# Kernel tuning notes

Measured on AMD Instinct MI355X. Metric: run time of the kernel, lower is better.

## Reference

```python
import jax, jax.numpy as jnp
import numpy as np

IN, H, FC1, FC2, OUT = 3, 30, 64, 32, 1
B, T = 8192, 256


def _lstm_layer(xT, W_ih, W_hh, b_ih, b_hh):
    """xT: (T, B, Din). Returns (hidden sequence (T,B,H), final h (B,H)).
    PyTorch gate order: i, f, g, o."""
    # Precompute input contribution for all timesteps (one big GEMM).
    gx = jnp.einsum('tbd,gd->tbg', xT, W_ih) + b_ih + b_hh  # (T,B,4H)
    b = xT.shape[1]
    h0 = jnp.zeros((b, W_hh.shape[1]), xT.dtype)
    c0 = h0

    def step(carry, g):
        h, c = carry
        gates = g + h @ W_hh.T
        i, f, gg, o = jnp.split(gates, 4, axis=-1)
        i = jax.nn.sigmoid(i)
        f = jax.nn.sigmoid(f)
        gg = jnp.tanh(gg)
        o = jax.nn.sigmoid(o)
        c = f * c + i * gg
        h = o * jnp.tanh(c)
        return (h, c), h

    (h_n, _), ys = jax.lax.scan(step, (h0, c0), gx)
    return ys, h_n


def setup_inputs() -> dict:
    key = jax.random.key(0)
    ks = jax.random.split(key, 16)
    s = 0.18  # ~1/sqrt(hidden_size), matches PyTorch uniform init scale
    inp = {
        'x': jax.random.normal(ks[0], (B, T, IN), jnp.float32),
        'W_ih0': jax.random.normal(ks[1], (4 * H, IN), jnp.float32) * s,
        'W_hh0': jax.random.normal(ks[2], (4 * H, H), jnp.float32) * s,
        'b_ih0': jax.random.normal(ks[3], (4 * H,), jnp.float32) * s,
        'b_hh0': jax.random.normal(ks[4], (4 * H,), jnp.float32) * s,
        'W_ih1': jax.random.normal(ks[5], (4 * H, H), jnp.float32) * s,
        'W_hh1': jax.random.normal(ks[6], (4 * H, H), jnp.float32) * s,
        'b_ih1': jax.random.normal(ks[7], (4 * H,), jnp.float32) * s,
        'b_hh1': jax.random.normal(ks[8], (4 * H,), jnp.float32) * s,
        'W_fc1': jax.random.normal(ks[9], (FC1, H), jnp.float32) * s,
        'b_fc1': jax.random.normal(ks[10], (FC1,), jnp.float32) * s,
        'W_fc2': jax.random.normal(ks[11], (FC2, FC1), jnp.float32) * 0.125,
        'b_fc2': jax.random.normal(ks[12], (FC2,), jnp.float32) * 0.125,
        'W_fc3': jax.random.normal(ks[13], (OUT, FC2), jnp.float32) * 0.17,
        'b_fc3': jax.random.normal(ks[14], (OUT,), jnp.float32) * 0.17,
    }
    return inp


def reference(x, W_ih0, W_hh0, b_ih0, b_hh0, W_ih1, W_hh1, b_ih1, b_hh1,
              W_fc1, b_fc1, W_fc2, b_fc2, W_fc3, b_fc3):
    xT = jnp.swapaxes(x, 0, 1)  # (T,B,IN)
    ys, _ = _lstm_layer(xT, W_ih0, W_hh0, b_ih0, b_hh0)   # layer 0 sequence
    _, h_n = _lstm_layer(ys, W_ih1, W_hh1, b_ih1, b_hh1)  # layer 1 final h
    # FC head (dropout = identity in eval mode)
    z = jax.nn.relu(h_n @ W_fc1.T + b_fc1)
    z = jax.nn.relu(z @ W_fc2.T + b_fc2)
    z = jax.nn.sigmoid(z @ W_fc3.T + b_fc3)
    return z.squeeze(-1)  # (B,)
```

## Files before the change

### kernel.cpp

```cpp
#include <hip/hip_runtime.h>

#define TT   256
#define HID  30
#define LOG2E 1.4426950408889634f
#define HS   40

typedef __bf16 bf16x8_t __attribute__((ext_vector_type(8)));
typedef float  f32x4_t  __attribute__((ext_vector_type(4)));

__device__ __forceinline__ float fexp2(float x){
#if __has_builtin(__builtin_amdgcn_exp2f)
    return __builtin_amdgcn_exp2f(x);
#else
    return exp2f(x);
#endif
}
__device__ __forceinline__ float frcp(float x){
#if __has_builtin(__builtin_amdgcn_rcpf)
    return __builtin_amdgcn_rcpf(x);
#else
    return 1.f/x;
#endif
}
__device__ __forceinline__ float fsigmoid(float x){ return frcp(1.f + fexp2(-LOG2E*x)); }
__device__ __forceinline__ f32x4_t exp4(f32x4_t v){
    f32x4_t e; e[0]=fexp2(v[0]); e[1]=fexp2(v[1]); e[2]=fexp2(v[2]); e[3]=fexp2(v[3]); return e;
}
__device__ __forceinline__ f32x4_t rcp4(f32x4_t v){
    f32x4_t r; r[0]=frcp(v[0]); r[1]=frcp(v[1]); r[2]=frcp(v[2]); r[3]=frcp(v[3]); return r;
}
__device__ __forceinline__ f32x4_t splat4(float v){ f32x4_t r = {v,v,v,v}; return r; }

__device__ __forceinline__ f32x4_t lstm_act(f32x4_t aI, f32x4_t aF, f32x4_t aG,
                                            f32x4_t aO, f32x4_t& cst){
    f32x4_t eI = exp4(aI);
    f32x4_t eF = exp4(aF);
    f32x4_t eG = exp4(aG);
    f32x4_t eO = exp4(aO);
    f32x4_t D1 = eF + 1.f;
    f32x4_t tG = eG + 1.f;
    f32x4_t D2 = eI*tG + tG;
    f32x4_t r  = rcp4(D1*D2);
    f32x4_t f  = r*D2;
    f32x4_t p  = (eG - 1.f) * (r*D1);
    cst = f*cst + p;
    f32x4_t cc;
    cc[0]=fminf(fmaxf(cst[0],-30.f),30.f);
    cc[1]=fminf(fmaxf(cst[1],-30.f),30.f);
    cc[2]=fminf(fmaxf(cst[2],-30.f),30.f);
    cc[3]=fminf(fmaxf(cst[3],-30.f),30.f);
    f32x4_t eC = exp4(cc * (2.f*LOG2E));
    f32x4_t tC = eC + 1.f;
    f32x4_t dn = eO*tC + tC;
    return (eC - 1.f) * rcp4(dn);
}

__global__ __launch_bounds__(256, 2)
void lstm_fused(const float* __restrict__ x,
    const float* __restrict__ Wih0, const float* __restrict__ Whh0,
    const float* __restrict__ bih0, const float* __restrict__ bhh0,
    const float* __restrict__ Wih1, const float* __restrict__ Whh1,
    const float* __restrict__ bih1, const float* __restrict__ bhh1,
    const float* __restrict__ Wfc1, const float* __restrict__ bfc1,
    const float* __restrict__ Wfc2, const float* __restrict__ bfc2,
    const float* __restrict__ Wfc3, const float* __restrict__ bfc3,
    float* __restrict__ out)
{
    __shared__ __align__(16) __bf16 h0f[2][16][HS];
    __shared__ __align__(16) __bf16 h1f[2][16][HS];
    __shared__ float h1_last[16*32];
    __shared__ float zbuf[16*64];
    __shared__ float z2buf[16*32];

    const int tid  = threadIdx.x;
    const int lane = tid & 63;
    const int wv   = tid >> 6;
    const int lay  = wv >> 1;
    const int uh   = wv & 1;
    const int n    = lane & 15;
    const int q    = lane >> 4;
    const int q4   = q*4;
    const int u    = uh*16 + n;
    const bool colok = (u < HID);
    const int uq   = colok ? u : 0;
    const int bbase = blockIdx.x * 16;

    bf16x8_t fA[4], fB[4];
    float bv[4], wx[4];
    {
        const float scl[4] = {-LOG2E, -LOG2E, 2.f*LOG2E, -LOG2E};
        #pragma unroll
        for (int g = 0; g < 4; ++g) {
            const int row = g*HID + uq;
            const float sg = scl[g];
            bf16x8_t va{}, vb{};
            #pragma unroll
            for (int j = 0; j < 8; ++j) {
                int k = q*8 + j;
                float a = 0.f, b = 0.f;
                if (colok) {
                    if (lay == 0) {
                        if (k < HID)      a = Whh0[row*HID + k];
                        else if (k < 32)  a = Wih0[row*3 + (k - HID)];
                    } else {
                        if (k < HID) { a = Wih1[row*HID + k];  b = Whh1[row*HID + k]; }
                    }
                }
                va[j] = (__bf16)(sg*a);
                vb[j] = (__bf16)(sg*b);
            }
            fA[g] = va;  fB[g] = vb;
            float bb = 0.f, ww = 0.f;
            if (colok) {
                bb = lay ? (bih1[row] + bhh1[row]) : (bih0[row] + bhh0[row]);
                if (lay == 0) ww = Wih0[row*3 + 2];
            }
            bv[g] = sg*bb;  wx[g] = sg*ww;
        }
    }

    f32x4_t cst = {0.f,0.f,0.f,0.f};

    for (int i = tid; i < 2*16*HS; i += 256) {
        (&h0f[0][0][0])[i] = (__bf16)0.f;
        (&h1f[0][0][0])[i] = (__bf16)0.f;
    }
    __syncthreads();
    if (tid < 32) {
        int m = tid >> 1, cc = tid & 1;
        h0f[1][m][30+cc] = (__bf16)x[(size_t)(bbase+m)*(TT*3) + cc];
    }
    __syncthreads();

    if (blockIdx.x & 256) {
        __builtin_amdgcn_s_sleep(16);
    }

    const float* xB = x + (size_t)bbase*(TT*3);
    const int xo2  = q4*(TT*3) + 2;
    const int xo01 = (((tid>>1)&15))*(TT*3) + (tid&1);
    f32x4_t x2 = {0.f,0.f,0.f,0.f};
    if (lay == 0) {
        x2[0]=xB[xo2]; x2[1]=xB[xo2+TT*3]; x2[2]=xB[xo2+2*TT*3]; x2[3]=xB[xo2+3*TT*3];
    }

#define STEP(S, RB, WB, FIRST) do {                                            \
    if (lay == 0) {                                                            \
        bf16x8_t A0 = *(const bf16x8_t*)(&h0f[RB][n][q*8]);                    \
        f32x4_t aI = __builtin_amdgcn_mfma_f32_16x16x32_bf16(A0, fA[0], x2*wx[0] + bv[0], 0,0,0); \
        f32x4_t aF = __builtin_amdgcn_mfma_f32_16x16x32_bf16(A0, fA[1], x2*wx[1] + bv[1], 0,0,0); \
        f32x4_t aG = __builtin_amdgcn_mfma_f32_16x16x32_bf16(A0, fA[2], x2*wx[2] + bv[2], 0,0,0); \
        f32x4_t aO = __builtin_amdgcn_mfma_f32_16x16x32_bf16(A0, fA[3], x2*wx[3] + bv[3], 0,0,0); \
        const int tpre = ((S)+2 < TT) ? (S)+2 : TT-1;                          \
        const float* xs = xB + 3*tpre;                                         \
        f32x4_t x2n;                                                           \
        x2n[0]=xs[xo2]; x2n[1]=xs[xo2+TT*3];                                   \
        x2n[2]=xs[xo2+2*TT*3]; x2n[3]=xs[xo2+3*TT*3];                          \
        float x01v = xs[xo01];                                                 \
        f32x4_t h = lstm_act(aI, aF, aG, aO, cst);                             \
        if (colok) {                                                           \
            h0f[WB][q4  ][u] = (__bf16)h[0];                                   \
            h0f[WB][q4+1][u] = (__bf16)h[1];                                   \
            h0f[WB][q4+2][u] = (__bf16)h[2];                                   \
            h0f[WB][q4+3][u] = (__bf16)h[3];                                   \
        }                                                                      \
        h0f[WB][(tid>>1)&15][30+(tid&1)] = (__bf16)x01v;                       \
        x2 = x2n;                                                              \
    } else if (!(FIRST)) {                                                     \
        bf16x8_t A1 = *(const bf16x8_t*)(&h0f[RB][n][q*8]);                    \
        bf16x8_t A2 = *(const bf16x8_t*)(&h1f[RB][n][q*8]);                    \
        f32x4_t aI = __builtin_amdgcn_mfma_f32_16x16x32_bf16(A2, fB[0], splat4(bv[0]), 0,0,0); \
        aI         = __builtin_amdgcn_mfma_f32_16x16x32_bf16(A1, fA[0], aI, 0,0,0); \
        f32x4_t aF = __builtin_amdgcn_mfma_f32_16x16x32_bf16(A2, fB[1], splat4(bv[1]), 0,0,0); \
        aF         = __builtin_amdgcn_mfma_f32_16x16x32_bf16(A1, fA[1], aF, 0,0,0); \
        f32x4_t aG = __builtin_amdgcn_mfma_f32_16x16x32_bf16(A2, fB[2], splat4(bv[2]), 0,0,0); \
        aG         = __builtin_amdgcn_mfma_f32_16x16x32_bf16(A1, fA[2], aG, 0,0,0); \
        f32x4_t aO = __builtin_amdgcn_mfma_f32_16x16x32_bf16(A2, fB[3], splat4(bv[3]), 0,0,0); \
        aO         = __builtin_amdgcn_mfma_f32_16x16x32_bf16(A1, fA[3], aO, 0,0,0); \
        f32x4_t h = lstm_act(aI, aF, aG, aO, cst);                             \
        h1f[WB][q4  ][u & 31] = (__bf16)h[0];                                  \
        h1f[WB][q4+1][u & 31] = (__bf16)h[1];                                  \
        h1f[WB][q4+2][u & 31] = (__bf16)h[2];                                  \
        h1f[WB][q4+3][u & 31] = (__bf16)h[3];                                  \
        if ((S) == TT-1) {                                                     \
            h1_last[(q4  )*32 + (u & 31)] = h[0];                              \
            h1_last[(q4+1)*32 + (u & 31)] = h[1];                              \
            h1_last[(q4+2)*32 + (u & 31)] = h[2];                              \
            h1_last[(q4+3)*32 + (u & 31)] = h[3];                              \
        }                                                                      \
    }                                                                          \
    __syncthreads();                                                           \
} while (0)

    STEP(-1, 1, 0, 1);
    #pragma unroll 1
    for (int s = 0; s < TT; s += 2) {
        STEP(s,   0, 1, 0);
        STEP(s+1, 1, 0, 0);
    }
#undef STEP

    #pragma unroll
    for (int rep = 0; rep < 4; ++rep) {
        int idx = tid + rep*256;
        int m = idx >> 6, uu = idx & 63;
        float a = bfc1[uu];
        for (int k = 0; k < HID; ++k) a += h1_last[m*32+k] * Wfc1[uu*HID+k];
        zbuf[m*64+uu] = fmaxf(a, 0.f);
    }
    __syncthreads();
    #pragma unroll
    for (int rep = 0; rep < 2; ++rep) {
        int idx = tid + rep*256;
        int m = idx >> 5, v = idx & 31;
        float a = bfc2[v];
        for (int k = 0; k < 64; ++k) a += zbuf[m*64+k] * Wfc2[v*64+k];
        z2buf[m*32+v] = fmaxf(a, 0.f);
    }
    __syncthreads();
    if (tid < 16) {
        float a = bfc3[0];
        for (int k = 0; k < 32; ++k) a += z2buf[tid*32+k] * Wfc3[k];
        out[bbase + tid] = fsigmoid(a);
    }
}

extern "C" void kernel_launch(void* const* d_in, const int* in_sizes, int n_in,
                              void* d_out, int out_size, void* d_ws, size_t ws_size,
                              hipStream_t stream) {
    const float* x    = (const float*)d_in[0];
    const float* Wih0 = (const float*)d_in[1];
    const float* Whh0 = (const float*)d_in[2];
    const float* bih0 = (const float*)d_in[3];
    const float* bhh0 = (const float*)d_in[4];
    const float* Wih1 = (const float*)d_in[5];
    const float* Whh1 = (const float*)d_in[6];
    const float* bih1 = (const float*)d_in[7];
    const float* bhh1 = (const float*)d_in[8];
    const float* Wfc1 = (const float*)d_in[9];
    const float* bfc1 = (const float*)d_in[10];
    const float* Wfc2 = (const float*)d_in[11];
    const float* bfc2 = (const float*)d_in[12];
    const float* Wfc3 = (const float*)d_in[13];
    const float* bfc3 = (const float*)d_in[14];
    float* outp = (float*)d_out;

    hipLaunchKernelGGL(lstm_fused, dim3(512), dim3(256), 0, stream,
        x, Wih0, Whh0, bih0, bhh0, Wih1, Whh1, bih1, bhh1,
        Wfc1, bfc1, Wfc2, bfc2, Wfc3, bfc3, outp);
}
```

Baseline: 275.8 us.

## Stage per-block input sequence in LDS and compute input projection in fp32

Each block now copies its whole 16×256×3 input slice into a 48 KB shared-memory buffer at kernel start. Layer 0 reads each step's inputs from LDS and computes the input-weight contribution in fp32 on the vector units, instead of doing per-step global loads and packing two input columns into the bf16 MFMA operand. This takes global-memory latency out of the serial recurrence and keeps the input term at full precision. The launch-stagger sleep is also removed. In exchange it adds a non-overlapped prologue load, extra VALU FMAs per step, and much more LDS per block, which may limit how many blocks fit on a CU.

New measurement: 272.6 us. No clear change (-1.2%).

```diff
diff --git a/kernel.cpp b/kernel.cpp
--- a/kernel.cpp
+++ b/kernel.cpp
@@ -66,6 +66,7 @@
     const float* __restrict__ Wfc3, const float* __restrict__ bfc3,
     float* __restrict__ out)
 {
+    __shared__ __align__(16) float  xlds[TT][48];
     __shared__ __align__(16) __bf16 h0f[2][16][HS];
     __shared__ __align__(16) __bf16 h1f[2][16][HS];
     __shared__ float h1_last[16*32];
@@ -86,7 +87,7 @@
     const int bbase = blockIdx.x * 16;
 
     bf16x8_t fA[4], fB[4];
-    float bv[4], wx[4];
+    float bv[4], wxv[4][3];
     {
         const float scl[4] = {-LOG2E, -LOG2E, 2.f*LOG2E, -LOG2E};
         #pragma unroll
@@ -98,24 +99,26 @@
             for (int j = 0; j < 8; ++j) {
                 int k = q*8 + j;
                 float a = 0.f, b = 0.f;
-                if (colok) {
-                    if (lay == 0) {
-                        if (k < HID)      a = Whh0[row*HID + k];
-                        else if (k < 32)  a = Wih0[row*3 + (k - HID)];
-                    } else {
-                        if (k < HID) { a = Wih1[row*HID + k];  b = Whh1[row*HID + k]; }
-                    }
+                if (colok && k < HID) {
+                    if (lay == 0) { a = Whh0[row*HID + k]; }
+                    else          { a = Wih1[row*HID + k];  b = Whh1[row*HID + k]; }
                 }
                 va[j] = (__bf16)(sg*a);
                 vb[j] = (__bf16)(sg*b);
             }
             fA[g] = va;  fB[g] = vb;
-            float bb = 0.f, ww = 0.f;
+            float bb = 0.f;
+            float w0 = 0.f, w1 = 0.f, w2 = 0.f;
             if (colok) {
                 bb = lay ? (bih1[row] + bhh1[row]) : (bih0[row] + bhh0[row]);
-                if (lay == 0) ww = Wih0[row*3 + 2];
+                if (lay == 0) {
+                    w0 = Wih0[row*3 + 0];
+                    w1 = Wih0[row*3 + 1];
+                    w2 = Wih0[row*3 + 2];
+                }
             }
-            bv[g] = sg*bb;  wx[g] = sg*ww;
+            bv[g] = sg*bb;
+            wxv[g][0] = sg*w0;  wxv[g][1] = sg*w1;  wxv[g][2] = sg*w2;
         }
     }
 
@@ -125,47 +128,52 @@
         (&h0f[0][0][0])[i] = (__bf16)0.f;
         (&h1f[0][0][0])[i] = (__bf16)0.f;
     }
+    {
+        const float* xg = x + (size_t)bbase*(TT*3);
+        for (int i4 = tid*4; i4 < 16*TT*3; i4 += 256*4) {
+            int row = i4 / (TT*3), tc0 = i4 % (TT*3);
+            f32x4_t v = *(const f32x4_t*)(xg + (size_t)row*(TT*3) + tc0);
+            #pragma unroll
+            for (int j = 0; j < 4; ++j) {
+                int tc = tc0 + j;
+                xlds[tc/3][row*3 + tc%3] = v[j];
+            }
+        }
+    }
     __syncthreads();
-    if (tid < 32) {
-        int m = tid >> 1, cc = tid & 1;
-        h0f[1][m][30+cc] = (__bf16)x[(size_t)(bbase+m)*(TT*3) + cc];
-    }
-    __syncthreads();
-
-    if (blockIdx.x & 256) {
-        __builtin_amdgcn_s_sleep(16);
-    }
-
-    const float* xB = x + (size_t)bbase*(TT*3);
-    const int xo2  = q4*(TT*3) + 2;
-    const int xo01 = (((tid>>1)&15))*(TT*3) + (tid&1);
-    f32x4_t x2 = {0.f,0.f,0.f,0.f};
-    if (lay == 0) {
-        x2[0]=xB[xo2]; x2[1]=xB[xo2+TT*3]; x2[2]=xB[xo2+2*TT*3]; x2[3]=xB[xo2+3*TT*3];
-    }
 
 #define STEP(S, RB, WB, FIRST) do {                                            \
     if (lay == 0) {                                                            \
+        const int tcur = ((S)+1 < TT) ? (S)+1 : TT-1;                          \
+        const float* xt = &xlds[tcur][q4*3];                                   \
+        f32x4_t xv0 = *(const f32x4_t*)(xt);          \
+        f32x4_t xv1 = *(const f32x4_t*)(xt + 4);      \
+        f32x4_t xv2 = *(const f32x4_t*)(xt + 8);      \
         bf16x8_t A0 = *(const bf16x8_t*)(&h0f[RB][n][q*8]);                    \
-        f32x4_t aI = __builtin_amdgcn_mfma_f32_16x16x32_bf16(A0, fA[0], x2*wx[0] + bv[0], 0,0,0); \
-        f32x4_t aF = __builtin_amdgcn_mfma_f32_16x16x32_bf16(A0, fA[1], x2*wx[1] + bv[1], 0,0,0); \
-        f32x4_t aG = __builtin_amdgcn_mfma_f32_16x16x32_bf16(A0, fA[2], x2*wx[2] + bv[2], 0,0,0); \
-        f32x4_t aO = __builtin_amdgcn_mfma_f32_16x16x32_bf16(A0, fA[3], x2*wx[3] + bv[3], 0,0,0); \
-        const int tpre = ((S)+2 < TT) ? (S)+2 : TT-1;                          \
-        const float* xs = xB + 3*tpre;                                         \
-        f32x4_t x2n;                                                           \
-        x2n[0]=xs[xo2]; x2n[1]=xs[xo2+TT*3];                                   \
-        x2n[2]=xs[xo2+2*TT*3]; x2n[3]=xs[xo2+3*TT*3];                          \
-        float x01v = xs[xo01];                                                 \
+        float xr[12];                                                          \
+        xr[0]=xv0[0]; xr[1]=xv0[1]; xr[2]=xv0[2]; xr[3]=xv0[3];                \
+        xr[4]=xv1[0]; xr[5]=xv1[1]; xr[6]=xv1[2]; xr[7]=xv1[3];                \
+        xr[8]=xv2[0]; xr[9]=xv2[1]; xr[10]=xv2[2]; xr[11]=xv2[3];              \
+        f32x4_t cin[4];                                                        \
+        _Pragma("unroll")                                                      \
+        for (int g = 0; g < 4; ++g) {                                          \
+            f32x4_t c;                                                         \
+            _Pragma("unroll")                                                  \
+            for (int r2 = 0; r2 < 4; ++r2)                                     \
+                c[r2] = bv[g] + wxv[g][0]*xr[3*r2]                             \
+                              + wxv[g][1]*xr[3*r2+1]                           \
+                              + wxv[g][2]*xr[3*r2+2];                          \
+            cin[g] = c;                                                        \
+        }                                                                      \
+        f32x4_t aI = __builtin_amdgcn_mfma_f32_16x16x32_bf16(A0, fA[0], cin[0], 0,0,0); \
+        f32x4_t aF = __builtin_amdgcn_mfma_f32_16x16x32_bf16(A0, fA[1], cin[1], 0,0,0); \
+        f32x4_t aG = __builtin_amdgcn_mfma_f32_16x16x32_bf16(A0, fA[2], cin[2], 0,0,0); \
+        f32x4_t aO = __builtin_amdgcn_mfma_f32_16x16x32_bf16(A0, fA[3], cin[3], 0,0,0); \
         f32x4_t h = lstm_act(aI, aF, aG, aO, cst);                             \
-        if (colok) {                                                           \
-            h0f[WB][q4  ][u] = (__bf16)h[0];                                   \
-            h0f[WB][q4+1][u] = (__bf16)h[1];                                   \
-            h0f[WB][q4+2][u] = (__bf16)h[2];                                   \
-            h0f[WB][q4+3][u] = (__bf16)h[3];                                   \
-        }                                                                      \
-        h0f[WB][(tid>>1)&15][30+(tid&1)] = (__bf16)x01v;                       \
-        x2 = x2n;                                                              \
+        h0f[WB][q4  ][u] = (__bf16)h[0];                                       \
+        h0f[WB][q4+1][u] = (__bf16)h[1];                                       \
+        h0f[WB][q4+2][u] = (__bf16)h[2];                                       \
+        h0f[WB][q4+3][u] = (__bf16)h[3];                                       \
     } else if (!(FIRST)) {                                                     \
         bf16x8_t A1 = *(const bf16x8_t*)(&h0f[RB][n][q*8]);                    \
         bf16x8_t A2 = *(const bf16x8_t*)(&h1f[RB][n][q*8]);                    \
```

## Replace block barriers with per-team flag handoff between LSTM layers via LDS ring

Applied to the files above, without the earlier changes.

Each block now handles 32 batch rows split into two teams. Within a team, one wave runs layer 0 and another runs layer 1, and they hand off through a 4-slot LDS ring of layer-0 hidden states with acquire/release flags instead of a __syncthreads per step. Each wave now computes all 30 hidden units itself (two MFMA column chunks), so no cross-wave exchange is needed within a layer. The whole x slice is staged into LDS up front, and the grid is halved to 256 blocks at one block per CU. The trade is less wave-level parallelism per CU and spin-waiting, in exchange for removing barrier latency and letting layer 0 run up to several steps ahead of layer 1.

Measured after the change: 330.6 us. 19.8% more time.

```diff
diff --git a/kernel.cpp b/kernel.cpp
--- a/kernel.cpp
+++ b/kernel.cpp
@@ -4,6 +4,7 @@
 #define HID  30
 #define LOG2E 1.4426950408889634f
 #define HS   40
+#define NS   4
 
 typedef __bf16 bf16x8_t __attribute__((ext_vector_type(8)));
 typedef float  f32x4_t  __attribute__((ext_vector_type(4)));
@@ -30,6 +31,13 @@
     f32x4_t r; r[0]=frcp(v[0]); r[1]=frcp(v[1]); r[2]=frcp(v[2]); r[3]=frcp(v[3]); return r;
 }
 __device__ __forceinline__ f32x4_t splat4(float v){ f32x4_t r = {v,v,v,v}; return r; }
+
+__device__ __forceinline__ int ld_acq(int* p){
+    return __hip_atomic_load(p, __ATOMIC_ACQUIRE, __HIP_MEMORY_SCOPE_WORKGROUP);
+}
+__device__ __forceinline__ void st_rel(int* p, int v){
+    __hip_atomic_store(p, v, __ATOMIC_RELEASE, __HIP_MEMORY_SCOPE_WORKGROUP);
+}
 
 __device__ __forceinline__ f32x4_t lstm_act(f32x4_t aI, f32x4_t aF, f32x4_t aG,
                                             f32x4_t aO, f32x4_t& cst){
@@ -55,7 +63,7 @@
     return (eC - 1.f) * rcp4(dn);
 }
 
-__global__ __launch_bounds__(256, 2)
+__global__ __launch_bounds__(256, 1)
 void lstm_fused(const float* __restrict__ x,
     const float* __restrict__ Wih0, const float* __restrict__ Whh0,
     const float* __restrict__ bih0, const float* __restrict__ bhh0,
@@ -66,161 +74,225 @@
     const float* __restrict__ Wfc3, const float* __restrict__ bfc3,
     float* __restrict__ out)
 {
-    __shared__ __align__(16) __bf16 h0f[2][16][HS];
-    __shared__ __align__(16) __bf16 h1f[2][16][HS];
-    __shared__ float h1_last[16*32];
-    __shared__ float zbuf[16*64];
-    __shared__ float z2buf[16*32];
+    __shared__ __align__(16) float  xlds2[TT][32];
+    __shared__ __align__(16) __bf16 xlds01[TT][32][2];
+    __shared__ __align__(16) __bf16 h0s[2][NS][16][HS];
+    __shared__ __align__(16) __bf16 h1s[2][16][HS];
+    __shared__ float h1_last[32][32];
+    __shared__ float zbuf[32][64];
+    __shared__ float z2buf[32][32];
+    __shared__ int   flags[2][2];
 
     const int tid  = threadIdx.x;
     const int lane = tid & 63;
     const int wv   = tid >> 6;
-    const int lay  = wv >> 1;
-    const int uh   = wv & 1;
+    const int role = wv >> 1;
+    const int team = wv & 1;
     const int n    = lane & 15;
     const int q    = lane >> 4;
     const int q4   = q*4;
-    const int u    = uh*16 + n;
-    const bool colok = (u < HID);
-    const int uq   = colok ? u : 0;
-    const int bbase = blockIdx.x * 16;
-
-    bf16x8_t fA[4], fB[4];
-    float bv[4], wx[4];
+    const int t16  = team*16;
+    const int bbase = blockIdx.x * 32;
+
+    bf16x8_t fA[4][2], fB[4][2];
+    float bvv[4][2], wxv[4][2];
     {
         const float scl[4] = {-LOG2E, -LOG2E, 2.f*LOG2E, -LOG2E};
         #pragma unroll
         for (int g = 0; g < 4; ++g) {
-            const int row = g*HID + uq;
-            const float sg = scl[g];
-            bf16x8_t va{}, vb{};
             #pragma unroll
-            for (int j = 0; j < 8; ++j) {
-                int k = q*8 + j;
-                float a = 0.f, b = 0.f;
-                if (colok) {
-                    if (lay == 0) {
-                        if (k < HID)      a = Whh0[row*HID + k];
-                        else if (k < 32)  a = Wih0[row*3 + (k - HID)];
-                    } else {
-                        if (k < HID) { a = Wih1[row*HID + k];  b = Whh1[row*HID + k]; }
+            for (int ch = 0; ch < 2; ++ch) {
+                const int u = ch*16 + n;
+                const bool ok = (u < HID);
+                const int uq = ok ? u : 0;
+                const int row = g*HID + uq;
+                const float sg = scl[g];
+                bf16x8_t va{}, vb{};
+                #pragma unroll
+                for (int j = 0; j < 8; ++j) {
+                    int k = q*8 + j;
+                    float a = 0.f, b = 0.f;
+                    if (ok) {
+                        if (role == 0) {
+                            if (k < HID)       a = Whh0[row*HID + k];
+                            else if (k == 30)  a = Wih0[row*3 + 0];
+                            else if (k == 31)  a = Wih0[row*3 + 1];
+                        } else {
+                            if (k < HID) { a = Wih1[row*HID + k];  b = Whh1[row*HID + k]; }
+                        }
                     }
+                    va[j] = (__bf16)(sg*a);
+                    vb[j] = (__bf16)(sg*b);
                 }
-                va[j] = (__bf16)(sg*a);
-                vb[j] = (__bf16)(sg*b);
+                fA[g][ch] = va;  fB[g][ch] = vb;
+                float bb = 0.f, ww = 0.f;
+                if (ok) {
+                    bb = role ? (bih1[row] + bhh1[row]) : (bih0[row] + bhh0[row]);
+                    if (role == 0) ww = Wih0[row*3 + 2];
+                }
+                bvv[g][ch] = sg*bb;
+                wxv[g][ch] = sg*ww;
             }
-            fA[g] = va;  fB[g] = vb;
-            float bb = 0.f, ww = 0.f;
-            if (colok) {
-                bb = lay ? (bih1[row] + bhh1[row]) : (bih0[row] + bhh0[row]);
-                if (lay == 0) ww = Wih0[row*3 + 2];
+        }
+    }
+
+    for (int i = tid; i < 2*NS*16*HS/2; i += 256)
+        ((uint32_t*)&h0s[0][0][0][0])[i] = 0u;
+    for (int i = tid; i < 2*16*HS/2; i += 256)
+        ((uint32_t*)&h1s[0][0][0])[i] = 0u;
+    {
+        const float* xg = x + (size_t)bbase*(TT*3);
+        for (int i4 = tid*4; i4 < 32*TT*3; i4 += 256*4) {
+            int row = i4 / (TT*3), tc0 = i4 % (TT*3);
+            f32x4_t v = *(const f32x4_t*)(xg + (size_t)row*(TT*3) + tc0);
+            #pragma unroll
+            for (int j = 0; j < 4; ++j) {
+                int tc = tc0 + j;
+                int t = tc/3, c = tc - 3*t;
+                if (c == 2) xlds2[t][row] = v[j];
+                else        xlds01[t][row][c] = (__bf16)v[j];
             }
-            bv[g] = sg*bb;  wx[g] = sg*ww;
         }
     }
-
-    f32x4_t cst = {0.f,0.f,0.f,0.f};
-
-    for (int i = tid; i < 2*16*HS; i += 256) {
-        (&h0f[0][0][0])[i] = (__bf16)0.f;
-        (&h1f[0][0][0])[i] = (__bf16)0.f;
-    }
+    if (tid == 0) { flags[0][0]=0; flags[0][1]=0; flags[1][0]=0; flags[1][1]=0; }
     __syncthreads();
-    if (tid < 32) {
-        int m = tid >> 1, cc = tid & 1;
-        h0f[1][m][30+cc] = (__bf16)x[(size_t)(bbase+m)*(TT*3) + cc];
-    }
-    __syncthreads();
-
-    if (blockIdx.x & 256) {
-        __builtin_amdgcn_s_sleep(16);
-    }
-
-    const float* xB = x + (size_t)bbase*(TT*3);
-    const int xo2  = q4*(TT*3) + 2;
-    const int xo01 = (((tid>>1)&15))*(TT*3) + (tid&1);
-    f32x4_t x2 = {0.f,0.f,0.f,0.f};
-    if (lay == 0) {
-        x2[0]=xB[xo2]; x2[1]=xB[xo2+TT*3]; x2[2]=xB[xo2+2*TT*3]; x2[3]=xB[xo2+3*TT*3];
-    }
-
-#define STEP(S, RB, WB, FIRST) do {                                            \
-    if (lay == 0) {                                                            \
-        bf16x8_t A0 = *(const bf16x8_t*)(&h0f[RB][n][q*8]);                    \
-        f32x4_t aI = __builtin_amdgcn_mfma_f32_16x16x32_bf16(A0, fA[0], x2*wx[0] + bv[0], 0,0,0); \
-        f32x4_t aF = __builtin_amdgcn_mfma_f32_16x16x32_bf16(A0, fA[1], x2*wx[1] + bv[1], 0,0,0); \
-        f32x4_t aG = __builtin_amdgcn_mfma_f32_16x16x32_bf16(A0, fA[2], x2*wx[2] + bv[2], 0,0,0); \
-        f32x4_t aO = __builtin_amdgcn_mfma_f32_16x16x32_bf16(A0, fA[3], x2*wx[3] + bv[3], 0,0,0); \
-        const int tpre = ((S)+2 < TT) ? (S)+2 : TT-1;                          \
-        const float* xs = xB + 3*tpre;                                         \
-        f32x4_t x2n;                                                           \
-        x2n[0]=xs[xo2]; x2n[1]=xs[xo2+TT*3];                                   \
-        x2n[2]=xs[xo2+2*TT*3]; x2n[3]=xs[xo2+3*TT*3];                          \
-        float x01v = xs[xo01];                                                 \
-        f32x4_t h = lstm_act(aI, aF, aG, aO, cst);                             \
-        if (colok) {                                                           \
-            h0f[WB][q4  ][u] = (__bf16)h[0];                                   \
-            h0f[WB][q4+1][u] = (__bf16)h[1];                                   \
-            h0f[WB][q4+2][u] = (__bf16)h[2];                                   \
-            h0f[WB][q4+3][u] = (__bf16)h[3];                                   \
-        }                                                                      \
-        h0f[WB][(tid>>1)&15][30+(tid&1)] = (__bf16)x01v;                       \
-        x2 = x2n;                                                              \
-    } else if (!(FIRST)) {                                                     \
-        bf16x8_t A1 = *(const bf16x8_t*)(&h0f[RB][n][q*8]);                    \
-        bf16x8_t A2 = *(const bf16x8_t*)(&h1f[RB][n][q*8]);                    \
-        f32x4_t aI = __builtin_amdgcn_mfma_f32_16x16x32_bf16(A2, fB[0], splat4(bv[0]), 0,0,0); \
-        aI         = __builtin_amdgcn_mfma_f32_16x16x32_bf16(A1, fA[0], aI, 0,0,0); \
-        f32x4_t aF = __builtin_amdgcn_mfma_f32_16x16x32_bf16(A2, fB[1], splat4(bv[1]), 0,0,0); \
-        aF         = __builtin_amdgcn_mfma_f32_16x16x32_bf16(A1, fA[1], aF, 0,0,0); \
-        f32x4_t aG = __builtin_amdgcn_mfma_f32_16x16x32_bf16(A2, fB[2], splat4(bv[2]), 0,0,0); \
-        aG         = __builtin_amdgcn_mfma_f32_16x16x32_bf16(A1, fA[2], aG, 0,0,0); \
-        f32x4_t aO = __builtin_amdgcn_mfma_f32_16x16x32_bf16(A2, fB[3], splat4(bv[3]), 0,0,0); \
-        aO         = __builtin_amdgcn_mfma_f32_16x16x32_bf16(A1, fA[3], aO, 0,0,0); \
-        f32x4_t h = lstm_act(aI, aF, aG, aO, cst);                             \
-        h1f[WB][q4  ][u & 31] = (__bf16)h[0];                                  \
-        h1f[WB][q4+1][u & 31] = (__bf16)h[1];                                  \
-        h1f[WB][q4+2][u & 31] = (__bf16)h[2];                                  \
-        h1f[WB][q4+3][u & 31] = (__bf16)h[3];                                  \
-        if ((S) == TT-1) {                                                     \
-            h1_last[(q4  )*32 + (u & 31)] = h[0];                              \
-            h1_last[(q4+1)*32 + (u & 31)] = h[1];                              \
-            h1_last[(q4+2)*32 + (u & 31)] = h[2];                              \
-            h1_last[(q4+3)*32 + (u & 31)] = h[3];                              \
+
+    if (role == 0) {
+        f32x4_t cstA = {0,0,0,0}, cstB = {0,0,0,0};
+        int consv = 0;
+        if (lane < 16)
+            *(uint32_t*)&h0s[team][NS-1][lane][30] = *(const uint32_t*)&xlds01[0][t16+lane][0];
+        f32x4_t  x2   = *(const f32x4_t*)&xlds2[0][t16 + q4];
+        uint32_t x01v = *(const uint32_t*)&xlds01[1][t16 + (lane & 15)][0];
+
+#define STEP_L0(T, RS, WS) do {                                                \
+    bf16x8_t A0 = *(const bf16x8_t*)&h0s[team][RS][n][q*8];                    \
+    f32x4_t aI0 = __builtin_amdgcn_mfma_f32_16x16x32_bf16(A0, fA[0][0], splat4(bvv[0][0]) + x2*wxv[0][0], 0,0,0); \
+    f32x4_t aF0 = __builtin_amdgcn_mfma_f32_16x16x32_bf16(A0, fA[1][0], splat4(bvv[1][0]) + x2*wxv[1][0], 0,0,0); \
+    f32x4_t aG0 = __builtin_amdgcn_mfma_f32_16x16x32_bf16(A0, fA[2][0], splat4(bvv[2][0]) + x2*wxv[2][0], 0,0,0); \
+    f32x4_t aO0 = __builtin_amdgcn_mfma_f32_16x16x32_bf16(A0, fA[3][0], splat4(bvv[3][0]) + x2*wxv[3][0], 0,0,0); \
+    f32x4_t aI1 = __builtin_amdgcn_mfma_f32_16x16x32_bf16(A0, fA[0][1], splat4(bvv[0][1]) + x2*wxv[0][1], 0,0,0); \
+    f32x4_t aF1 = __builtin_amdgcn_mfma_f32_16x16x32_bf16(A0, fA[1][1], splat4(bvv[1][1]) + x2*wxv[1][1], 0,0,0); \
+    f32x4_t aG1 = __builtin_amdgcn_mfma_f32_16x16x32_bf16(A0, fA[2][1], splat4(bvv[2][1]) + x2*wxv[2][1], 0,0,0); \
+    f32x4_t aO1 = __builtin_amdgcn_mfma_f32_16x16x32_bf16(A0, fA[3][1], splat4(bvv[3][1]) + x2*wxv[3][1], 0,0,0); \
+    f32x4_t hA = lstm_act(aI0, aF0, aG0, aO0, cstA);                           \
+    f32x4_t hB = lstm_act(aI1, aF1, aG1, aO1, cstB);                           \
+    h0s[team][WS][q4  ][n] = (__bf16)hA[0];                                    \
+    h0s[team][WS][q4+1][n] = (__bf16)hA[1];                                    \
+    h0s[team][WS][q4+2][n] = (__bf16)hA[2];                                    \
+    h0s[team][WS][q4+3][n] = (__bf16)hA[3];                                    \
+    if (n < 14) {                                                              \
+        h0s[team][WS][q4  ][16+n] = (__bf16)hB[0];                             \
+        h0s[team][WS][q4+1][16+n] = (__bf16)hB[1];                             \
+        h0s[team][WS][q4+2][16+n] = (__bf16)hB[2];                             \
+        h0s[team][WS][q4+3][16+n] = (__bf16)hB[3];                             \
+    }                                                                          \
+    if (lane < 16) *(uint32_t*)&h0s[team][WS][lane][30] = x01v;                \
+    if (lane == 0) st_rel(&flags[team][0], (T)+1);                             \
+    if ((T)+1 >= NS) {                                                         \
+        while (consv < (T)-(NS-2)) consv = ld_acq(&flags[team][1]);            \
+    }                                                                          \
+    { int tn = ((T)+2 < TT) ? (T)+2 : TT-1;                                    \
+      x01v = *(const uint32_t*)&xlds01[tn][t16 + (lane & 15)][0]; }            \
+    { int tx = ((T)+1 < TT) ? (T)+1 : TT-1;                                    \
+      x2 = *(const f32x4_t*)&xlds2[tx][t16 + q4]; }                            \
+} while (0)
+
+        #pragma unroll 1
+        for (int it = 0; it < TT/4; ++it) {
+            const int T0 = it*4;
+            STEP_L0(T0+0, 3, 0);
+            STEP_L0(T0+1, 0, 1);
+            STEP_L0(T0+2, 1, 2);
+            STEP_L0(T0+3, 2, 3);
+        }
+#undef STEP_L0
+    } else {
+        f32x4_t cstA = {0,0,0,0}, cstB = {0,0,0,0};
+        int seqv = 0;
+
+#define STEP_L1(T, SLOT, LAST) do {                                            \
+    while (seqv < (T)+1) seqv = ld_acq(&flags[team][0]);                       \
+    bf16x8_t A1 = *(const bf16x8_t*)&h0s[team][SLOT][n][q*8];                  \
+    bf16x8_t A2 = *(const bf16x8_t*)&h1s[team][n][q*8];                        \
+    if (lane == 0) st_rel(&flags[team][1], (T)+1);                             \
+    f32x4_t aI0 = __builtin_amdgcn_mfma_f32_16x16x32_bf16(A2, fB[0][0], splat4(bvv[0][0]), 0,0,0); \
+    f32x4_t aF0 = __builtin_amdgcn_mfma_f32_16x16x32_bf16(A2, fB[1][0], splat4(bvv[1][0]), 0,0,0); \
+    f32x4_t aG0 = __builtin_amdgcn_mfma_f32_16x16x32_bf16(A2, fB[2][0], splat4(bvv[2][0]), 0,0,0); \
+    f32x4_t aO0 = __builtin_amdgcn_mfma_f32_16x16x32_bf16(A2, fB[3][0], splat4(bvv[3][0]), 0,0,0); \
+    f32x4_t aI1 = __builtin_amdgcn_mfma_f32_16x16x32_bf16(A2, fB[0][1], splat4(bvv[0][1]), 0,0,0); \
+    f32x4_t aF1 = __builtin_amdgcn_mfma_f32_16x16x32_bf16(A2, fB[1][1], splat4(bvv[1][1]), 0,0,0); \
+    f32x4_t aG1 = __builtin_amdgcn_mfma_f32_16x16x32_bf16(A2, fB[2][1], splat4(bvv[2][1]), 0,0,0); \
+    f32x4_t aO1 = __builtin_amdgcn_mfma_f32_16x16x32_bf16(A2, fB[3][1], splat4(bvv[3][1]), 0,0,0); \
+    aI0 = __builtin_amdgcn_mfma_f32_16x16x32_bf16(A1, fA[0][0], aI0, 0,0,0);   \
+    aF0 = __builtin_amdgcn_mfma_f32_16x16x32_bf16(A1, fA[1][0], aF0, 0,0,0);   \
+    aG0 = __builtin_amdgcn_mfma_f32_16x16x32_bf16(A1, fA[2][0], aG0, 0,0,0);   \
+    aO0 = __builtin_amdgcn_mfma_f32_16x16x32_bf16(A1, fA[3][0], aO0, 0,0,0);   \
+    aI1 = __builtin_amdgcn_mfma_f32_16x16x32_bf16(A1, fA[0][1], aI1, 0,0,0);   \
+    aF1 = __builtin_amdgcn_mfma_f32_16x16x32_bf16(A1, fA[1][1], aF1, 0,0,0);   \
+    aG1 = __builtin_amdgcn_mfma_f32_16x16x32_bf16(A1, fA[2][1], aG1, 0,0,0);   \
+    aO1 = __builtin_amdgcn_mfma_f32_16x16x32_bf16(A1, fA[3][1], aO1, 0,0,0);   \
+    f32x4_t hA = lstm_act(aI0, aF0, aG0, aO0, cstA);                           \
+    f32x4_t hB = lstm_act(aI1, aF1, aG1, aO1, cstB);                           \
+    h1s[team][q4  ][n] = (__bf16)hA[0];                                        \
+    h1s[team][q4+1][n] = (__bf16)hA[1];                                        \
+    h1s[team][q4+2][n] = (__bf16)hA[2];                                        \
+    h1s[team][q4+3][n] = (__bf16)hA[3];                                        \
+    if (n < 14) {                                                              \
+        h1s[team][q4  ][16+n] = (__bf16)hB[0];                                 \
+        h1s[team][q4+1][16+n] = (__bf16)hB[1];                                 \
+        h1s[team][q4+2][16+n] = (__bf16)hB[2];                                 \
+        h1s[team][q4+3][16+n] = (__bf16)hB[3];                                 \
+    }                                                                          \
+    if (LAST) {                                                                \
+        h1_last[t16+q4  ][n] = hA[0];                                          \
+        h1_last[t16+q4+1][n] = hA[1];                                          \
+        h1_last[t16+q4+2][n] = hA[2];                                          \
+        h1_last[t16+q4+3][n] = hA[3];                                          \
+        if (n < 14) {                                                          \
+            h1_last[t16+q4  ][16+n] = hB[0];                                   \
+            h1_last[t16+q4+1][16+n] = hB[1];                                   \
+            h1_last[t16+q4+2][16+n] = hB[2];                                   \
+            h1_last[t16+q4+3][16+n] = hB[3];                                   \
         }                                                                      \
     }                                                                          \
-    __syncthreads();                                                           \
+    seqv = ld_acq(&flags[team][0]);                                            \
 } while (0)
 
-    STEP(-1, 1, 0, 1);
-    #pragma unroll 1
-    for (int s = 0; s < TT; s += 2) {
-        STEP(s,   0, 1, 0);
-        STEP(s+1, 1, 0, 0);
-    }
-#undef STEP
-
+        #pragma unroll 1
+        for (int it = 0; it < TT/4; ++it) {
+            const int T0 = it*4;
+            STEP_L1(T0+0, 0, 0);
+            STEP_L1(T0+1, 1, 0);
+            STEP_L1(T0+2, 2, 0);
+            STEP_L1(T0+3, 3, (it == TT/4 - 1));
+        }
+#undef STEP_L1
+    }
+
+    __syncthreads();
+
+    #pragma unroll
+    for (int rep = 0; rep < 8; ++rep) {
+        int idx = tid + rep*256;
+        int m = idx >> 6, uu = idx & 63;
+        float a = bfc1[uu];
+        for (int k = 0; k < HID; ++k) a += h1_last[m][k] * Wfc1[uu*HID+k];
+        zbuf[m][uu] = fmaxf(a, 0.f);
+    }
+    __syncthreads();
     #pragma unroll
     for (int rep = 0; rep < 4; ++rep) {
         int idx = tid + rep*256;
-        int m = idx >> 6, uu = idx & 63;
-        float a = bfc1[uu];
-        for (int k = 0; k < HID; ++k) a += h1_last[m*32+k] * Wfc1[uu*HID+k];
-        zbuf[m*64+uu] = fmaxf(a, 0.f);
-    }
-    __syncthreads();
-    #pragma unroll
-    for (int rep = 0; rep < 2; ++rep) {
-        int idx = tid + rep*256;
         int m = idx >> 5, v = idx & 31;
         float a = bfc2[v];
-        for (int k = 0; k < 64; ++k) a += zbuf[m*64+k] * Wfc2[v*64+k];
-        z2buf[m*32+v] = fmaxf(a, 0.f);
+        for (int k = 0; k < 64; ++k) a += zbuf[m][k] * Wfc2[v*64+k];
+        z2buf[m][v] = fmaxf(a, 0.f);
     }
     __syncthreads();
-    if (tid < 16) {
+    if (tid < 32) {
         float a = bfc3[0];
-        for (int k = 0; k < 32; ++k) a += z2buf[tid*32+k] * Wfc3[k];
+        for (int k = 0; k < 32; ++k) a += z2buf[tid][k] * Wfc3[k];
         out[bbase + tid] = fsigmoid(a);
     }
 }
@@ -245,7 +317,7 @@
     const float* bfc3 = (const float*)d_in[14];
     float* outp = (float*)d_out;
 
-    hipLaunchKernelGGL(lstm_fused, dim3(512), dim3(256), 0, stream,
+    hipLaunchKernelGGL(lstm_fused, dim3(256), dim3(256), 0, stream,
         x, Wih0, Whh0, bih0, bhh0, Wih1, Whh1, bih1, bhh1,
         Wfc1, bfc1, Wfc2, bfc2, Wfc3, bfc3, outp);
 }
```

## Run both LSTM layers in one wavefront with register-level hidden-state transposes

Applied to the files above, without the earlier changes.

Each block shrinks from four wavefronts (two layers by two unit halves) to a single wavefront that computes both layers and all 30 units. The hidden state is passed between timesteps in registers using ds_bpermute transposes and packed bf16 conversions, with the weights as the MFMA A operand, so the per-step shared-memory stores, loads and block barriers go away. Layer 1 now consumes the current step's layer-0 output in the same iteration instead of lagging one step. In exchange each wave does four times the MFMA and activation work serially, uses far more registers, and runs only 512 waves on the device, so latency hiding depends on ILP within a wave.

Measured after the change: 406.3 us. 1.47x slower.

```diff
diff --git a/kernel.cpp b/kernel.cpp
--- a/kernel.cpp
+++ b/kernel.cpp
@@ -3,10 +3,10 @@
 #define TT   256
 #define HID  30
 #define LOG2E 1.4426950408889634f
-#define HS   40
 
 typedef __bf16 bf16x8_t __attribute__((ext_vector_type(8)));
 typedef float  f32x4_t  __attribute__((ext_vector_type(4)));
+typedef unsigned int u32x4_t __attribute__((ext_vector_type(4)));
 
 __device__ __forceinline__ float fexp2(float x){
 #if __has_builtin(__builtin_amdgcn_exp2f)
@@ -29,7 +29,12 @@
 __device__ __forceinline__ f32x4_t rcp4(f32x4_t v){
     f32x4_t r; r[0]=frcp(v[0]); r[1]=frcp(v[1]); r[2]=frcp(v[2]); r[3]=frcp(v[3]); return r;
 }
-__device__ __forceinline__ f32x4_t splat4(float v){ f32x4_t r = {v,v,v,v}; return r; }
+
+__device__ __forceinline__ uint32_t pk_bf16(float lo, float hi){
+    uint32_t r;
+    asm("v_cvt_pk_bf16_f32 %0, %1, %2" : "=v"(r) : "v"(lo), "v"(hi));
+    return r;
+}
 
 __device__ __forceinline__ f32x4_t lstm_act(f32x4_t aI, f32x4_t aF, f32x4_t aG,
                                             f32x4_t aO, f32x4_t& cst){
@@ -55,7 +60,7 @@
     return (eC - 1.f) * rcp4(dn);
 }
 
-__global__ __launch_bounds__(256, 2)
+__global__ __launch_bounds__(64, 1)
 void lstm_fused(const float* __restrict__ x,
     const float* __restrict__ Wih0, const float* __restrict__ Whh0,
     const float* __restrict__ bih0, const float* __restrict__ bhh0,
@@ -66,162 +71,169 @@
     const float* __restrict__ Wfc3, const float* __restrict__ bfc3,
     float* __restrict__ out)
 {
-    __shared__ __align__(16) __bf16 h0f[2][16][HS];
-    __shared__ __align__(16) __bf16 h1f[2][16][HS];
-    __shared__ float h1_last[16*32];
-    __shared__ float zbuf[16*64];
-    __shared__ float z2buf[16*32];
-
-    const int tid  = threadIdx.x;
-    const int lane = tid & 63;
-    const int wv   = tid >> 6;
-    const int lay  = wv >> 1;
-    const int uh   = wv & 1;
+    __shared__ float h1_last[16][32];
+    __shared__ float zbuf[16][64];
+    __shared__ float z2buf[16][32];
+
+    const int lane = threadIdx.x;
     const int n    = lane & 15;
     const int q    = lane >> 4;
     const int q4   = q*4;
-    const int u    = uh*16 + n;
-    const bool colok = (u < HID);
-    const int uq   = colok ? u : 0;
     const int bbase = blockIdx.x * 16;
 
-    bf16x8_t fA[4], fB[4];
-    float bv[4], wx[4];
+    bf16x8_t w0[4][2], wi1[4][2], wh1[4][2];
+    f32x4_t  bq0[4][2], wxq[4][2], bq1[4][2];
     {
         const float scl[4] = {-LOG2E, -LOG2E, 2.f*LOG2E, -LOG2E};
         #pragma unroll
         for (int g = 0; g < 4; ++g) {
-            const int row = g*HID + uq;
-            const float sg = scl[g];
-            bf16x8_t va{}, vb{};
             #pragma unroll
-            for (int j = 0; j < 8; ++j) {
-                int k = q*8 + j;
-                float a = 0.f, b = 0.f;
-                if (colok) {
-                    if (lay == 0) {
-                        if (k < HID)      a = Whh0[row*HID + k];
-                        else if (k < 32)  a = Wih0[row*3 + (k - HID)];
-                    } else {
-                        if (k < HID) { a = Wih1[row*HID + k];  b = Whh1[row*HID + k]; }
+            for (int ch = 0; ch < 2; ++ch) {
+                const float sg = scl[g];
+                {
+                    const int uf = ch*16 + n;
+                    const int uq = (uf < HID) ? uf : 0;
+                    const int row = g*HID + uq;
+                    bf16x8_t a{}, b{}, c{};
+                    #pragma unroll
+                    for (int j = 0; j < 8; ++j) {
+                        const int k = q*8 + j;
+                        float va=0.f, vb=0.f, vc=0.f;
+                        if (k < HID) {
+                            va = Whh0[row*HID + k];
+                            vb = Wih1[row*HID + k];
+                            vc = Whh1[row*HID + k];
+                        } else if (k == 30) { va = Wih0[row*3 + 0]; }
+                        else                { va = Wih0[row*3 + 1]; }
+                        a[j]=(__bf16)(sg*va); b[j]=(__bf16)(sg*vb); c[j]=(__bf16)(sg*vc);
                     }
+                    w0[g][ch]=a; wi1[g][ch]=b; wh1[g][ch]=c;
                 }
-                va[j] = (__bf16)(sg*a);
-                vb[j] = (__bf16)(sg*b);
+                f32x4_t b0v, wxv, b1v;
+                #pragma unroll
+                for (int r = 0; r < 4; ++r) {
+                    const int ub = ch*16 + q4 + r;
+                    const int uq = (ub < HID) ? ub : 0;
+                    const int row = g*HID + uq;
+                    b0v[r] = sg*(bih0[row] + bhh0[row]);
+                    wxv[r] = sg*Wih0[row*3 + 2];
+                    b1v[r] = sg*(bih1[row] + bhh1[row]);
+                }
+                bq0[g][ch]=b0v; wxq[g][ch]=wxv; bq1[g][ch]=b1v;
             }
-            fA[g] = va;  fB[g] = vb;
-            float bb = 0.f, ww = 0.f;
-            if (colok) {
-                bb = lay ? (bih1[row] + bhh1[row]) : (bih0[row] + bhh0[row]);
-                if (lay == 0) ww = Wih0[row*3 + 2];
-            }
-            bv[g] = sg*bb;  wx[g] = sg*ww;
         }
     }
 
-    f32x4_t cst = {0.f,0.f,0.f,0.f};
-
-    for (int i = tid; i < 2*16*HS; i += 256) {
-        (&h0f[0][0][0])[i] = (__bf16)0.f;
-        (&h1f[0][0][0])[i] = (__bf16)0.f;
-    }
+    const float* xr = x + (size_t)(bbase + n) * (TT*3);
+    float px0[4], px1[4], px2[4];
+    #pragma unroll
+    for (int i = 0; i < 4; ++i) { px0[i]=xr[3*i]; px1[i]=xr[3*i+1]; px2[i]=xr[3*i+2]; }
+
+    const int  ad01 = 4*(n + 32*(q & 1));
+    const int  ad23 = ad01 + 64;
+    const bool qlo  = (q < 2);
+    const bool q3   = (q == 3);
+
+    bf16x8_t h0frag, h1frag;
+    {
+        u32x4_t z = {0u,0u,0u,0u};
+        if (q3) z[3] = pk_bf16(px0[0], px1[0]);
+        h0frag = __builtin_bit_cast(bf16x8_t, z);
+        u32x4_t z1 = {0u,0u,0u,0u};
+        h1frag = __builtin_bit_cast(bf16x8_t, z1);
+    }
+    f32x4_t c0A={0,0,0,0}, c0B={0,0,0,0}, c1A={0,0,0,0}, c1B={0,0,0,0};
+
+#define MF(A,B,C) __builtin_amdgcn_mfma_f32_16x16x32_bf16((A),(B),(C),0,0,0)
+#define BP(a,s)   ((uint32_t)__builtin_amdgcn_ds_bpermute((a),(int)(s)))
+
+#define XPOSE(hA, hB, XW, dst) do {                                            \
+    uint32_t a01=pk_bf16((hA)[0],(hA)[1]), a23=pk_bf16((hA)[2],(hA)[3]);       \
+    uint32_t b01=pk_bf16((hB)[0],(hB)[1]), b23=pk_bf16((hB)[2],(hB)[3]);       \
+    uint32_t t0a=BP(ad01,a01), t1a=BP(ad01,a23), t2a=BP(ad23,a01), t3a=BP(ad23,a23); \
+    uint32_t t0b=BP(ad01,b01), t1b=BP(ad01,b23), t2b=BP(ad23,b01), t3b=BP(ad23,b23); \
+    u32x4_t fw;                                                                \
+    fw[0] = qlo ? t0a : t0b;                                                   \
+    fw[1] = qlo ? t1a : t1b;                                                   \
+    fw[2] = qlo ? t2a : t2b;                                                   \
+    fw[3] = q3 ? (XW) : (qlo ? t3a : t3b);                                     \
+    (dst) = __builtin_bit_cast(bf16x8_t, fw);                                  \
+} while (0)
+
+#define STEP(S, SA, SB) do {                                                   \
+    const float x2v = px2[SA];                                                 \
+                                \
+    f32x4_t aI0 = MF(w0[0][0], h0frag, bq0[0][0] + wxq[0][0]*x2v);             \
+    f32x4_t aF0 = MF(w0[1][0], h0frag, bq0[1][0] + wxq[1][0]*x2v);             \
+    f32x4_t aG0 = MF(w0[2][0], h0frag, bq0[2][0] + wxq[2][0]*x2v);             \
+    f32x4_t aO0 = MF(w0[3][0], h0frag, bq0[3][0] + wxq[3][0]*x2v);             \
+    f32x4_t aI1 = MF(w0[0][1], h0frag, bq0[0][1] + wxq[0][1]*x2v);             \
+    f32x4_t aF1 = MF(w0[1][1], h0frag, bq0[1][1] + wxq[1][1]*x2v);             \
+    f32x4_t aG1 = MF(w0[2][1], h0frag, bq0[2][1] + wxq[2][1]*x2v);             \
+    f32x4_t aO1 = MF(w0[3][1], h0frag, bq0[3][1] + wxq[3][1]*x2v);             \
+     \
+    f32x4_t dI0 = MF(wh1[0][0], h1frag, bq1[0][0]);                            \
+    f32x4_t dF0 = MF(wh1[1][0], h1frag, bq1[1][0]);                            \
+    f32x4_t dG0 = MF(wh1[2][0], h1frag, bq1[2][0]);                            \
+    f32x4_t dO0 = MF(wh1[3][0], h1frag, bq1[3][0]);                            \
+    f32x4_t dI1 = MF(wh1[0][1], h1frag, bq1[0][1]);                            \
+    f32x4_t dF1 = MF(wh1[1][1], h1frag, bq1[1][1]);                            \
+    f32x4_t dG1 = MF(wh1[2][1], h1frag, bq1[2][1]);                            \
+    f32x4_t dO1 = MF(wh1[3][1], h1frag, bq1[3][1]);                            \
+    f32x4_t h0A = lstm_act(aI0,aF0,aG0,aO0,c0A);                               \
+    f32x4_t h0B = lstm_act(aI1,aF1,aG1,aO1,c0B);                               \
+    XPOSE(h0A, h0B, pk_bf16(px0[SB], px1[SB]), h0frag);    \
+               \
+    dI0 = MF(wi1[0][0], h0frag, dI0);  dF0 = MF(wi1[1][0], h0frag, dF0);       \
+    dG0 = MF(wi1[2][0], h0frag, dG0);  dO0 = MF(wi1[3][0], h0frag, dO0);       \
+    dI1 = MF(wi1[0][1], h0frag, dI1);  dF1 = MF(wi1[1][1], h0frag, dF1);       \
+    dG1 = MF(wi1[2][1], h0frag, dG1);  dO1 = MF(wi1[3][1], h0frag, dO1);       \
+    f32x4_t h1A = lstm_act(dI0,dF0,dG0,dO0,c1A);                               \
+    f32x4_t h1B = lstm_act(dI1,dF1,dG1,dO1,c1B);                               \
+    if ((S) == TT-1) {                                                         \
+        *(f32x4_t*)&h1_last[n][q4]    = h1A;                                   \
+        *(f32x4_t*)&h1_last[n][16+q4] = h1B;                                   \
+    } else {                                                                   \
+        XPOSE(h1A, h1B, 0u, h1frag);                                           \
+    }                                                                          \
+    { const int tp = ((S)+4 < TT) ? (S)+4 : TT-1;                              \
+      px0[SA]=xr[3*tp]; px1[SA]=xr[3*tp+1]; px2[SA]=xr[3*tp+2]; }              \
+} while (0)
+
+    #pragma unroll 1
+    for (int s = 0; s < TT; s += 4) {
+        STEP(s+0, 0, 1);
+        STEP(s+1, 1, 2);
+        STEP(s+2, 2, 3);
+        STEP(s+3, 3, 0);
+    }
+#undef STEP
+#undef XPOSE
+#undef BP
+#undef MF
+
     __syncthreads();
-    if (tid < 32) {
-        int m = tid >> 1, cc = tid & 1;
-        h0f[1][m][30+cc] = (__bf16)x[(size_t)(bbase+m)*(TT*3) + cc];
+
+    #pragma unroll 1
+    for (int m = 0; m < 16; ++m) {
+        float a = bfc1[lane];
+        for (int k = 0; k < HID; ++k) a += h1_last[m][k] * Wfc1[lane*HID+k];
+        zbuf[m][lane] = fmaxf(a, 0.f);
     }
     __syncthreads();
-
-    if (blockIdx.x & 256) {
-        __builtin_amdgcn_s_sleep(16);
-    }
-
-    const float* xB = x + (size_t)bbase*(TT*3);
-    const int xo2  = q4*(TT*3) + 2;
-    const int xo01 = (((tid>>1)&15))*(TT*3) + (tid&1);
-    f32x4_t x2 = {0.f,0.f,0.f,0.f};
-    if (lay == 0) {
-        x2[0]=xB[xo2]; x2[1]=xB[xo2+TT*3]; x2[2]=xB[xo2+2*TT*3]; x2[3]=xB[xo2+3*TT*3];
-    }
-
-#define STEP(S, RB, WB, FIRST) do {                                            \
-    if (lay == 0) {                                                            \
-        bf16x8_t A0 = *(const bf16x8_t*)(&h0f[RB][n][q*8]);                    \
-        f32x4_t aI = __builtin_amdgcn_mfma_f32_16x16x32_bf16(A0, fA[0], x2*wx[0] + bv[0], 0,0,0); \
-        f32x4_t aF = __builtin_amdgcn_mfma_f32_16x16x32_bf16(A0, fA[1], x2*wx[1] + bv[1], 0,0,0); \
-        f32x4_t aG = __builtin_amdgcn_mfma_f32_16x16x32_bf16(A0, fA[2], x2*wx[2] + bv[2], 0,0,0); \
-        f32x4_t aO = __builtin_amdgcn_mfma_f32_16x16x32_bf16(A0, fA[3], x2*wx[3] + bv[3], 0,0,0); \
-        const int tpre = ((S)+2 < TT) ? (S)+2 : TT-1;                          \
-        const float* xs = xB + 3*tpre;                                         \
-        f32x4_t x2n;                                                           \
-        x2n[0]=xs[xo2]; x2n[1]=xs[xo2+TT*3];                                   \
-        x2n[2]=xs[xo2+2*TT*3]; x2n[3]=xs[xo2+3*TT*3];                          \
-        float x01v = xs[xo01];                                                 \
-        f32x4_t h = lstm_act(aI, aF, aG, aO, cst);                             \
-        if (colok) {                                                           \
-            h0f[WB][q4  ][u] = (__bf16)h[0];                                   \
-            h0f[WB][q4+1][u] = (__bf16)h[1];                                   \
-            h0f[WB][q4+2][u] = (__bf16)h[2];                                   \
-            h0f[WB][q4+3][u] = (__bf16)h[3];                                   \
-        }                                                                      \
-        h0f[WB][(tid>>1)&15][30+(tid&1)] = (__bf16)x01v;                       \
-        x2 = x2n;                                                              \
-    } else if (!(FIRST)) {                                                     \
-        bf16x8_t A1 = *(const bf16x8_t*)(&h0f[RB][n][q*8]);                    \
-        bf16x8_t A2 = *(const bf16x8_t*)(&h1f[RB][n][q*8]);                    \
-        f32x4_t aI = __builtin_amdgcn_mfma_f32_16x16x32_bf16(A2, fB[0], splat4(bv[0]), 0,0,0); \
-        aI         = __builtin_amdgcn_mfma_f32_16x16x32_bf16(A1, fA[0], aI, 0,0,0); \
-        f32x4_t aF = __builtin_amdgcn_mfma_f32_16x16x32_bf16(A2, fB[1], splat4(bv[1]), 0,0,0); \
-        aF         = __builtin_amdgcn_mfma_f32_16x16x32_bf16(A1, fA[1], aF, 0,0,0); \
-        f32x4_t aG = __builtin_amdgcn_mfma_f32_16x16x32_bf16(A2, fB[2], splat4(bv[2]), 0,0,0); \
-        aG         = __builtin_amdgcn_mfma_f32_16x16x32_bf16(A1, fA[2], aG, 0,0,0); \
-        f32x4_t aO = __builtin_amdgcn_mfma_f32_16x16x32_bf16(A2, fB[3], splat4(bv[3]), 0,0,0); \
-        aO         = __builtin_amdgcn_mfma_f32_16x16x32_bf16(A1, fA[3], aO, 0,0,0); \
-        f32x4_t h = lstm_act(aI, aF, aG, aO, cst);                             \
-        h1f[WB][q4  ][u & 31] = (__bf16)h[0];                                  \
-        h1f[WB][q4+1][u & 31] = (__bf16)h[1];                                  \
-        h1f[WB][q4+2][u & 31] = (__bf16)h[2];                                  \
-        h1f[WB][q4+3][u & 31] = (__bf16)h[3];                                  \
-        if ((S) == TT-1) {                                                     \
-            h1_last[(q4  )*32 + (u & 31)] = h[0];                              \
-            h1_last[(q4+1)*32 + (u & 31)] = h[1];                              \
-            h1_last[(q4+2)*32 + (u & 31)] = h[2];                              \
-            h1_last[(q4+3)*32 + (u & 31)] = h[3];                              \
-        }                                                                      \
-    }                                                                          \
-    __syncthreads();                                                           \
-} while (0)
-
-    STEP(-1, 1, 0, 1);
     #pragma unroll 1
-    for (int s = 0; s < TT; s += 2) {
-        STEP(s,   0, 1, 0);
-        STEP(s+1, 1, 0, 0);
-    }
-#undef STEP
-
-    #pragma unroll
-    for (int rep = 0; rep < 4; ++rep) {
-        int idx = tid + rep*256;
-        int m = idx >> 6, uu = idx & 63;
-        float a = bfc1[uu];
-        for (int k = 0; k < HID; ++k) a += h1_last[m*32+k] * Wfc1[uu*HID+k];
-        zbuf[m*64+uu] = fmaxf(a, 0.f);
-    }
-    __syncthreads();
-    #pragma unroll
-    for (int rep = 0; rep < 2; ++rep) {
-        int idx = tid + rep*256;
+    for (int rep = 0; rep < 8; ++rep) {
+        int idx = lane + rep*64;
         int m = idx >> 5, v = idx & 31;
         float a = bfc2[v];
-        for (int k = 0; k < 64; ++k) a += zbuf[m*64+k] * Wfc2[v*64+k];
-        z2buf[m*32+v] = fmaxf(a, 0.f);
+        for (int k = 0; k < 64; ++k) a += zbuf[m][k] * Wfc2[v*64+k];
+        z2buf[m][v] = fmaxf(a, 0.f);
     }
     __syncthreads();
-    if (tid < 16) {
+    if (lane < 16) {
         float a = bfc3[0];
-        for (int k = 0; k < 32; ++k) a += z2buf[tid*32+k] * Wfc3[k];
-        out[bbase + tid] = fsigmoid(a);
+        for (int k = 0; k < 32; ++k) a += z2buf[lane][k] * Wfc3[k];
+        out[bbase + lane] = fsigmoid(a);
     }
 }
 
@@ -245,7 +257,7 @@
     const float* bfc3 = (const float*)d_in[14];
     float* outp = (float*)d_out;
 
-    hipLaunchKernelGGL(lstm_fused, dim3(512), dim3(256), 0, stream,
+    hipLaunchKernelGGL(lstm_fused, dim3(512), dim3(64), 0, stream,
         x, Wih0, Whh0, bih0, bhh0, Wih1, Whh1, bih1, bhh1,
         Wfc1, bfc1, Wfc2, bfc2, Wfc3, bfc3, outp);
 }
```
